# Kernel optimization log

Measured on AMD Instinct MI355X. Metric: run time of the kernel, lower is better.

Reference implementation:

```python
import jax, jax.numpy as jnp
from jax import lax
import numpy as np


def _qlayer(x, theta):
    """Simulate QLayer: RX(x_i) encoder + trainable RX(theta_i) per wire
    (they commute -> single RX(x_i+theta_i) on |0>), then ring of CNOTs,
    then <Z> on each wire.  x: (B, n) float, theta: (n,). Returns (B, n)."""
    B, n = x.shape
    a = x + theta[None, :]
    c = jnp.cos(a * 0.5)
    s = jnp.sin(a * 0.5)
    # RX(a)|0> = [cos(a/2), -i sin(a/2)] per wire -> product state
    amps = jnp.stack([c + 0j, -1j * s], axis=-1)  # (B, n, 2) complex64
    state = amps[:, 0]  # (B, 2)
    for w in range(1, n):
        state = state[..., None] * amps[:, w].reshape((B,) + (1,) * w + (2,))
    # state: (B, 2, 2, ..., 2), axis w+1 == wire w
    for ctrl in range(n):
        tgt = (ctrl + 1) % n
        s0 = jnp.take(state, 0, axis=ctrl + 1)   # control = 0 block
        s1 = jnp.take(state, 1, axis=ctrl + 1)   # control = 1 block
        t_ax = tgt + 1 if tgt < ctrl else tgt    # target axis after removing ctrl axis
        s1 = jnp.flip(s1, axis=t_ax)             # X on target
        state = jnp.stack([s0, s1], axis=ctrl + 1)
    p = state.real ** 2 + state.imag ** 2
    axes = tuple(range(1, n + 1))
    zs = []
    for w in range(n):
        other = tuple(ax for ax in axes if ax != w + 1)
        pw = jnp.sum(p, axis=other)              # (B, 2)
        zs.append(pw[:, 0] - pw[:, 1])           # <Z_w> = P(0) - P(1)
    return jnp.stack(zs, axis=1)


def setup_inputs() -> dict:
    key = jax.random.key(0)
    ks = jax.random.split(key, 13)
    T, B, D, NQ = 64, 256, 512, 6
    lim = 1.0 / np.sqrt(D + NQ)

    def lin(k):
        k1, k2 = jax.random.split(k)
        W = jax.random.uniform(k1, (D + NQ, NQ), jnp.float32, -lim, lim)
        b = jax.random.uniform(k2, (NQ,), jnp.float32, -lim, lim)
        return W, b

    Wf, bf = lin(ks[0]); Wi, bi = lin(ks[1]); Wu, bu = lin(ks[2]); Wo, bo = lin(ks[3])
    theta_f = jax.random.normal(ks[4], (NQ,), jnp.float32) * 0.1
    theta_i = jax.random.normal(ks[5], (NQ,), jnp.float32) * 0.1
    theta_u = jax.random.normal(ks[6], (NQ,), jnp.float32) * 0.1
    theta_o = jax.random.normal(ks[7], (NQ,), jnp.float32) * 0.1
    inputs = jax.random.normal(ks[8], (T, B, D), jnp.float32)
    return {"inputs": inputs,
            "Wf": Wf, "bf": bf, "Wi": Wi, "bi": bi,
            "Wu": Wu, "bu": bu, "Wo": Wo, "bo": bo,
            "theta_f": theta_f, "theta_i": theta_i,
            "theta_u": theta_u, "theta_o": theta_o}


def reference(inputs, Wf, bf, Wi, bi, Wu, bu, Wo, bo,
              theta_f, theta_i, theta_u, theta_o):
    B = inputs.shape[1]
    NQ = theta_f.shape[0]  # hidden_dim == n_qubits
    h0 = jnp.zeros((B, NQ), inputs.dtype)
    c0 = jnp.zeros((B, NQ), inputs.dtype)

    def step(carry, x):
        hx, cx = carry
        comb = jnp.concatenate([x, hx], axis=1)          # (B, D+NQ)
        f = jax.nn.sigmoid(_qlayer(comb @ Wf + bf, theta_f))
        i = jax.nn.sigmoid(_qlayer(comb @ Wi + bi, theta_i))
        g = jnp.tanh(_qlayer(comb @ Wu + bu, theta_u))
        o = jax.nn.sigmoid(_qlayer(comb @ Wo + bo, theta_o))
        cx2 = f * cx + i * g
        hx2 = o * jnp.tanh(cx2)
        return (hx2, cx2), hx2

    (hx, cx), outputs = lax.scan(step, (h0, c0), inputs)  # outputs: (T, B, NQ)
    return outputs, hx, cx
```

## Files before the change

kernel.cpp:

```cpp
#include <hip/hip_runtime.h>


__device__ __forceinline__ float fast_rcp(float x) { return __builtin_amdgcn_rcpf(x); }

__global__ __launch_bounds__(256) void gemm_pre(
    const float* __restrict__ X,
    const float* __restrict__ Wf, const float* __restrict__ bf,
    const float* __restrict__ Wi, const float* __restrict__ bi,
    const float* __restrict__ Wu, const float* __restrict__ bu,
    const float* __restrict__ Wo, const float* __restrict__ bo,
    const float* __restrict__ thf, const float* __restrict__ thi,
    const float* __restrict__ thu, const float* __restrict__ tho,
    float* __restrict__ pre)
{
    __shared__ float Buf[6144];
    __shared__ float Bs[24];

    const int tid = threadIdx.x;
    if (tid < 24) {
        int g = tid / 6, w = tid % 6;
        const float* bb = (g==0)?bf:(g==1)?bi:(g==2)?bu:bo;
        const float* tt = (g==0)?thf:(g==1)?thi:(g==2)?thu:tho;
        Bs[tid] = bb[w] + tt[w];
    }

    const int r    = tid & 63;
    const int ksub = tid >> 6;
    const int kuni = __builtin_amdgcn_readfirstlane(ksub << 4);
    const int rowbase = blockIdx.x * 64;

    float acc[24];
    #pragma unroll
    for (int j = 0; j < 24; ++j) acc[j] = 0.f;

    for (int kb = 0; kb < 512; kb += 64) {
        __syncthreads();
        #pragma unroll
        for (int i = 0; i < 4; ++i) {
            int f  = tid + i*256;
            int rr = f >> 4, k4 = f & 15;
            const float4 v = *(const float4*)(X + (rowbase + rr)*512 + kb + k4*4);
            *(float4*)(&Buf[rr*68 + k4*4]) = v;
        }
        __syncthreads();
        #pragma unroll
        for (int kk4 = 0; kk4 < 4; ++kk4) {
            float4 a4 = *(const float4*)(&Buf[r*68 + kuni + kk4*4]);
            float av[4] = {a4.x, a4.y, a4.z, a4.w};
            #pragma unroll
            for (int q = 0; q < 4; ++q) {
                const int k = kb + kuni + kk4*4 + q;
                const float a = av[q];
                #pragma unroll
                for (int gg = 0; gg < 4; ++gg) {
                    const float* Wp = (gg==0)?Wf:(gg==1)?Wi:(gg==2)?Wu:Wo;
                    const float2* pw = (const float2*)(Wp + k*6);
                    float2 w0 = pw[0], w1 = pw[1], w2 = pw[2];
                    acc[gg*6+0] = fmaf(a, w0.x, acc[gg*6+0]);
                    acc[gg*6+1] = fmaf(a, w0.y, acc[gg*6+1]);
                    acc[gg*6+2] = fmaf(a, w1.x, acc[gg*6+2]);
                    acc[gg*6+3] = fmaf(a, w1.y, acc[gg*6+3]);
                    acc[gg*6+4] = fmaf(a, w2.x, acc[gg*6+4]);
                    acc[gg*6+5] = fmaf(a, w2.y, acc[gg*6+5]);
                }
            }
        }
    }

    __syncthreads();
    {
        float4* dst = (float4*)&Buf[(ksub*64 + r)*24];
        dst[0] = make_float4(acc[0],  acc[1],  acc[2],  acc[3]);
        dst[1] = make_float4(acc[4],  acc[5],  acc[6],  acc[7]);
        dst[2] = make_float4(acc[8],  acc[9],  acc[10], acc[11]);
        dst[3] = make_float4(acc[12], acc[13], acc[14], acc[15]);
        dst[4] = make_float4(acc[16], acc[17], acc[18], acc[19]);
        dst[5] = make_float4(acc[20], acc[21], acc[22], acc[23]);
    }
    __syncthreads();
    #pragma unroll
    for (int i = 0; i < 6; ++i) {
        int f  = i*256 + tid;
        int rr = f / 24, j = f % 24;
        float s = Buf[rr*24 + j] + Buf[1536 + rr*24 + j]
                + Buf[3072 + rr*24 + j] + Buf[4608 + rr*24 + j] + Bs[j];
        pre[(rowbase + rr)*24 + j] = s;
    }
}

__global__ __launch_bounds__(64) void qlstm_scan(
    const float* __restrict__ pre,
    const float* __restrict__ Wf, const float* __restrict__ Wi,
    const float* __restrict__ Wu, const float* __restrict__ Wo,
    float* __restrict__ out)
{
    __shared__ float act_s[2][16][28];

    const int lane = threadIdx.x;
    const int bl   = lane >> 2;
    const int g    = lane & 3;
    const int b    = blockIdx.x * 16 + bl;

    const float* Wg = (g==0)?Wf:(g==1)?Wi:(g==2)?Wu:Wo;
    float Wh[6][6];
    #pragma unroll
    for (int j = 0; j < 6; ++j)
        #pragma unroll
        for (int w = 0; w < 6; ++w)
            Wh[j][w] = Wg[(512 + j)*6 + w];

    const float k1 = (g==2) ? 2.f : 1.f;
    const float k2 = (g==2) ? 2.f : 1.f;
    const float k3 = (g==2) ? -1.f : 0.f;

    float h[6], c[6];
    #pragma unroll
    for (int w = 0; w < 6; ++w) { h[w] = 0.f; c[w] = 0.f; }

    const float* p0 = pre + b*24 + g*6;
    float2 x0 = *(const float2*)(p0);
    float2 x1 = *(const float2*)(p0 + 2);
    float2 x2 = *(const float2*)(p0 + 4);

    for (int t = 0; t < 64; ++t) {
        float xw[6] = {x0.x, x0.y, x1.x, x1.y, x2.x, x2.y};
        int tn = (t < 63) ? (t + 1) : 63;
        const float* pn = pre + (tn*256 + b)*24 + g*6;
        x0 = *(const float2*)(pn);
        x1 = *(const float2*)(pn + 2);
        x2 = *(const float2*)(pn + 4);

        float a[6];
        #pragma unroll
        for (int w = 0; w < 6; ++w) a[w] = xw[w];
        #pragma unroll
        for (int j = 0; j < 6; ++j)
            #pragma unroll
            for (int w = 0; w < 6; ++w)
                a[w] = fmaf(h[j], Wh[j][w], a[w]);

        float C[6];
        #pragma unroll
        for (int w = 0; w < 6; ++w) C[w] = __cosf(a[w]);

        float z[6];
        z[1] = C[0]*C[1];
        z[2] = z[1]*C[2];
        z[3] = z[2]*C[3];
        z[4] = z[3]*C[4];
        z[5] = z[4]*C[5];
        z[0] = (C[1]*C[2])*((C[3]*C[4])*C[5]);

        float act[6];
        #pragma unroll
        for (int w = 0; w < 6; ++w) {
            float e = __expf(-k1 * z[w]);
            act[w] = fmaf(k2, fast_rcp(1.f + e), k3);
        }

        const int par = t & 1;
        float2* ap = (float2*)&act_s[par][bl][g*6];
        ap[0] = make_float2(act[0], act[1]);
        ap[1] = make_float2(act[2], act[3]);
        ap[2] = make_float2(act[4], act[5]);
        __syncthreads();

        const float4* Aq = (const float4*)&act_s[par][bl][0];
        float4 q0 = Aq[0], q1 = Aq[1], q2 = Aq[2], q3 = Aq[3], q4 = Aq[4], q5 = Aq[5];
        float F[6] = {q0.x, q0.y, q0.z, q0.w, q1.x, q1.y};
        float I[6] = {q1.z, q1.w, q2.x, q2.y, q2.z, q2.w};
        float U[6] = {q3.x, q3.y, q3.z, q3.w, q4.x, q4.y};
        float O[6] = {q4.z, q4.w, q5.x, q5.y, q5.z, q5.w};

        #pragma unroll
        for (int w = 0; w < 6; ++w) {
            c[w] = fmaf(F[w], c[w], I[w]*U[w]);
            float e  = __expf(-2.f * c[w]);
            float tc = fmaf(2.f, fast_rcp(1.f + e), -1.f);
            h[w] = O[w]*tc;
        }

        if (g < 3) {
            float2 v;
            v.x = (g==0) ? h[0] : (g==1) ? h[2] : h[4];
            v.y = (g==0) ? h[1] : (g==1) ? h[3] : h[5];
            *(float2*)(out + (t*256 + b)*6 + g*2) = v;
        }
    }

    if (g < 3) {
        float2 v;
        v.x = (g==0) ? h[0] : (g==1) ? h[2] : h[4];
        v.y = (g==0) ? h[1] : (g==1) ? h[3] : h[5];
        *(float2*)(out + 64*256*6 + b*6 + g*2) = v;
        float2 u;
        u.x = (g==0) ? c[0] : (g==1) ? c[2] : c[4];
        u.y = (g==0) ? c[1] : (g==1) ? c[3] : c[5];
        *(float2*)(out + 64*256*6 + 256*6 + b*6 + g*2) = u;
    }
}

extern "C" void kernel_launch(void* const* d_in, const int* in_sizes, int n_in,
                              void* d_out, int out_size, void* d_ws, size_t ws_size,
                              hipStream_t stream) {
    const float* X   = (const float*)d_in[0];
    const float* Wf  = (const float*)d_in[1];
    const float* bf_ = (const float*)d_in[2];
    const float* Wi  = (const float*)d_in[3];
    const float* bi_ = (const float*)d_in[4];
    const float* Wu  = (const float*)d_in[5];
    const float* bu_ = (const float*)d_in[6];
    const float* Wo  = (const float*)d_in[7];
    const float* bo_ = (const float*)d_in[8];
    const float* thf = (const float*)d_in[9];
    const float* thi = (const float*)d_in[10];
    const float* thu = (const float*)d_in[11];
    const float* tho = (const float*)d_in[12];

    float* pre = (float*)d_ws;
    float* out = (float*)d_out;

    gemm_pre<<<256, 256, 0, stream>>>(X, Wf, bf_, Wi, bi_, Wu, bu_, Wo, bo_,
                                      thf, thi, thu, tho, pre);
    qlstm_scan<<<16, 64, 0, stream>>>(pre, Wf, Wi, Wu, Wo, out);
}
```

Baseline: 151.5 us.

## Replace LDS exchange with quad swizzle broadcasts and prefetch X tiles in GEMM

In the scan kernel, each quad now shares its four gate activations through ds_swizzle quad broadcasts instead of writing them to shared memory and calling __syncthreads every timestep. This removes a barrier and the LDS round trip from the serial recurrence, at the cost of 24 swizzle instructions per step. The cosine product chain is also rebalanced into a shallower tree to shorten the dependency latency. The GEMM kernel now register-prefetches the next X tile while computing on the current one, overlapping global loads with FMAs.

```diff
diff --git a/kernel.cpp b/kernel.cpp
--- a/kernel.cpp
+++ b/kernel.cpp
@@ -2,6 +2,12 @@
 
 
 __device__ __forceinline__ float fast_rcp(float x) { return __builtin_amdgcn_rcpf(x); }
+
+template <int G>
+__device__ __forceinline__ float quad_bcast(float v) {
+    int i = __builtin_amdgcn_ds_swizzle(__float_as_int(v), 0x8000 | (G * 0x55));
+    return __int_as_float(i);
+}
 
 __global__ __launch_bounds__(256) void gemm_pre(
     const float* __restrict__ X,
@@ -29,20 +35,29 @@
     const int kuni = __builtin_amdgcn_readfirstlane(ksub << 4);
     const int rowbase = blockIdx.x * 64;
 
+    const int srow = tid >> 4;
+    const int sk4  = tid & 15;
+
     float acc[24];
     #pragma unroll
     for (int j = 0; j < 24; ++j) acc[j] = 0.f;
+
+    float4 pf[4];
+    #pragma unroll
+    for (int i = 0; i < 4; ++i)
+        pf[i] = *(const float4*)(X + (rowbase + srow + i*16)*512 + 0 + sk4*4);
 
     for (int kb = 0; kb < 512; kb += 64) {
         __syncthreads();
         #pragma unroll
-        for (int i = 0; i < 4; ++i) {
-            int f  = tid + i*256;
-            int rr = f >> 4, k4 = f & 15;
-            const float4 v = *(const float4*)(X + (rowbase + rr)*512 + kb + k4*4);
-            *(float4*)(&Buf[rr*68 + k4*4]) = v;
-        }
+        for (int i = 0; i < 4; ++i)
+            *(float4*)(&Buf[(srow + i*16)*68 + sk4*4]) = pf[i];
         __syncthreads();
+        if (kb < 448) {
+            #pragma unroll
+            for (int i = 0; i < 4; ++i)
+                pf[i] = *(const float4*)(X + (rowbase + srow + i*16)*512 + (kb + 64) + sk4*4);
+        }
         #pragma unroll
         for (int kk4 = 0; kk4 < 4; ++kk4) {
             float4 a4 = *(const float4*)(&Buf[r*68 + kuni + kk4*4]);
@@ -88,14 +103,12 @@
     }
 }
 
-__global__ __launch_bounds__(64) void qlstm_scan(
+__global__ __launch_bounds__(64, 1) void qlstm_scan(
     const float* __restrict__ pre,
     const float* __restrict__ Wf, const float* __restrict__ Wi,
     const float* __restrict__ Wu, const float* __restrict__ Wo,
     float* __restrict__ out)
 {
-    __shared__ float act_s[2][16][28];
-
     const int lane = threadIdx.x;
     const int bl   = lane >> 2;
     const int g    = lane & 3;
@@ -143,13 +156,14 @@
         #pragma unroll
         for (int w = 0; w < 6; ++w) C[w] = __cosf(a[w]);
 
+        float p01 = C[0]*C[1], p23 = C[2]*C[3], p45 = C[4]*C[5];
         float z[6];
-        z[1] = C[0]*C[1];
-        z[2] = z[1]*C[2];
-        z[3] = z[2]*C[3];
+        z[1] = p01;
+        z[2] = p01*C[2];
+        z[3] = p01*p23;
         z[4] = z[3]*C[4];
-        z[5] = z[4]*C[5];
-        z[0] = (C[1]*C[2])*((C[3]*C[4])*C[5]);
+        z[5] = z[3]*p45;
+        z[0] = C[1]*(p23*p45);
 
         float act[6];
         #pragma unroll
@@ -158,19 +172,14 @@
             act[w] = fmaf(k2, fast_rcp(1.f + e), k3);
         }
 
-        const int par = t & 1;
-        float2* ap = (float2*)&act_s[par][bl][g*6];
-        ap[0] = make_float2(act[0], act[1]);
-        ap[1] = make_float2(act[2], act[3]);
-        ap[2] = make_float2(act[4], act[5]);
-        __syncthreads();
-
-        const float4* Aq = (const float4*)&act_s[par][bl][0];
-        float4 q0 = Aq[0], q1 = Aq[1], q2 = Aq[2], q3 = Aq[3], q4 = Aq[4], q5 = Aq[5];
-        float F[6] = {q0.x, q0.y, q0.z, q0.w, q1.x, q1.y};
-        float I[6] = {q1.z, q1.w, q2.x, q2.y, q2.z, q2.w};
-        float U[6] = {q3.x, q3.y, q3.z, q3.w, q4.x, q4.y};
-        float O[6] = {q4.z, q4.w, q5.x, q5.y, q5.z, q5.w};
+        float F[6], I[6], U[6], O[6];
+        #pragma unroll
+        for (int w = 0; w < 6; ++w) {
+            F[w] = quad_bcast<0>(act[w]);
+            I[w] = quad_bcast<1>(act[w]);
+            U[w] = quad_bcast<2>(act[w]);
+            O[w] = quad_bcast<3>(act[w]);
+        }
 
         #pragma unroll
         for (int w = 0; w < 6; ++w) {
```

Result: slower. 160.1 us (+5.7%).
